# Optimization experiments

Hardware: AMD Instinct MI355X
Metric: run time of the kernel (lower is better)

The kernel has to match this reference:

```python
import jax, jax.numpy as jnp
import numpy as np

NUM_SPEC_CHARS = 2  # matches init_kwargs
VOCAB = 50000
EMBED = 128
B = 4096

def setup_inputs() -> dict:
    key = jax.random.key(0)
    k1, k2 = jax.random.split(key)
    input_ = jax.random.normal(k1, (B, VOCAB - NUM_SPEC_CHARS), dtype=jnp.float32)
    word2vecs = jax.random.normal(k2, (VOCAB, EMBED), dtype=jnp.float32)
    return {"input_": input_, "word2vecs": word2vecs}

def reference(input_, word2vecs):
    # forward: matmul of (b, vocab_eff) against table with special chars stripped
    table = word2vecs[:-NUM_SPEC_CHARS] if NUM_SPEC_CHARS > 0 else word2vecs
    return jnp.matmul(input_, table)  # (b, embed)
```

## Files before the change

kernel.cpp:

```cpp
#include <hip/hip_runtime.h>

#define M_ROWS 4096
#define K_EFF  49998
#define K_PAD  50048
#define N_EMB  128
#define BM     64
#define BK     64
#define S_SPLIT 16
#define IT_TOTAL 782
#define OUT_ELEMS (M_ROWS * N_EMB)

typedef __attribute__((ext_vector_type(8))) short        short8;
typedef __attribute__((ext_vector_type(4))) float        floatx4;
typedef __attribute__((ext_vector_type(2))) float        floatx2;
typedef __attribute__((ext_vector_type(4))) unsigned int uintx4;

__device__ __forceinline__ unsigned short f2bf(float f){
  unsigned int u = __builtin_bit_cast(unsigned int, f);
  u += 0x7fffu + ((u >> 16) & 1u);
  return (unsigned short)(u >> 16);
}

__global__ void prep_bt(const float* __restrict__ W,
                        unsigned short* __restrict__ Bt,
                        float* __restrict__ out){
  __shared__ unsigned short T[64 * 132];
  const int tid = threadIdx.x;

  const int gid = blockIdx.x * 256 + tid;
  if (gid < OUT_ELEMS / 4) ((floatx4*)out)[gid] = (floatx4)0.0f;

  const int kp0 = blockIdx.x * 64;

#pragma unroll
  for (int p = 0; p < 8; ++p){
    const int id = p * 256 + tid;
    const int r  = id >> 5;
    const int c4 = id & 31;
    const int kp = kp0 + r;
    floatx4 f = (floatx4)0.0f;
    if (kp < K_EFF) f = *(const floatx4*)(W + (size_t)kp * N_EMB + c4 * 4);
    const unsigned int u0 = f2bf(f.x) | ((unsigned)f2bf(f.y) << 16);
    const unsigned int u1 = f2bf(f.z) | ((unsigned)f2bf(f.w) << 16);
    *(unsigned int*)(&T[r * 132 + c4 * 4])     = u0;
    *(unsigned int*)(&T[r * 132 + c4 * 4 + 2]) = u1;
  }
  __syncthreads();

#pragma unroll
  for (int p = 0; p < 4; ++p){
    const int id = p * 256 + tid;
    const int n  = id >> 3;
    const int c  = id & 7;
    unsigned short v[8];
#pragma unroll
    for (int j = 0; j < 8; ++j) v[j] = T[(c * 8 + j) * 132 + n];
    uintx4 pk;
    pk.x = v[0] | ((unsigned)v[1] << 16);
    pk.y = v[2] | ((unsigned)v[3] << 16);
    pk.z = v[4] | ((unsigned)v[5] << 16);
    pk.w = v[6] | ((unsigned)v[7] << 16);
    *(uintx4*)(Bt + (size_t)n * K_PAD + kp0 + c * 8) = pk;
  }
}

__global__ void gemm_bf16_splitk(const float* __restrict__ A,
                                 const unsigned short* __restrict__ Bt,
                                 float* __restrict__ out){
  __shared__ unsigned short As[BM * 72];
  __shared__ unsigned short Bs[N_EMB * 72];

  const int tid   = threadIdx.x;
  const int bx    = blockIdx.x;
  const int mtile = bx & 63;
  const int s     = bx >> 6;
  const int m0    = mtile * BM;
  const int it0   = (s * IT_TOTAL) >> 4;
  const int it1   = ((s + 1) * IT_TOTAL) >> 4;

  const int lane = tid & 63;
  const int wv   = tid >> 6;
  const int col  = lane & 15;
  const int quad = lane >> 4;

  floatx4 acc[8];
#pragma unroll
  for (int c = 0; c < 8; ++c) acc[c] = (floatx4)0.0f;

  for (int it = it0; it < it1; ++it){
    const int kt = it * BK;
    __syncthreads();

    if (kt + BK <= K_EFF){
#pragma unroll
      for (int p = 0; p < 2; ++p){
        const int row = p * 32 + (tid >> 3);
        const int c   = tid & 7;
        const floatx2* src =
            (const floatx2*)(A + (size_t)(m0 + row) * K_EFF + kt + c * 8);
        floatx2 f0 = __builtin_nontemporal_load(src + 0);
        floatx2 f1 = __builtin_nontemporal_load(src + 1);
        floatx2 f2 = __builtin_nontemporal_load(src + 2);
        floatx2 f3 = __builtin_nontemporal_load(src + 3);
        uintx4 pk;
        pk.x = f2bf(f0.x) | ((unsigned)f2bf(f0.y) << 16);
        pk.y = f2bf(f1.x) | ((unsigned)f2bf(f1.y) << 16);
        pk.z = f2bf(f2.x) | ((unsigned)f2bf(f2.y) << 16);
        pk.w = f2bf(f3.x) | ((unsigned)f2bf(f3.y) << 16);
        *(uintx4*)(&As[row * 72 + c * 8]) = pk;
      }
    } else {
#pragma unroll
      for (int p = 0; p < 2; ++p){
        const int row = p * 32 + (tid >> 3);
        const int c   = tid & 7;
        const float* src = A + (size_t)(m0 + row) * K_EFF;
        unsigned short v[8];
#pragma unroll
        for (int j = 0; j < 8; ++j){
          const int k = kt + c * 8 + j;
          v[j] = (k < K_EFF) ? f2bf(src[k]) : (unsigned short)0;
        }
        uintx4 pk;
        pk.x = v[0] | ((unsigned)v[1] << 16);
        pk.y = v[2] | ((unsigned)v[3] << 16);
        pk.z = v[4] | ((unsigned)v[5] << 16);
        pk.w = v[6] | ((unsigned)v[7] << 16);
        *(uintx4*)(&As[row * 72 + c * 8]) = pk;
      }
    }

#pragma unroll
    for (int p = 0; p < 4; ++p){
      const int n = p * 32 + (tid >> 3);
      const int c = tid & 7;
      const uintx4 d = *(const uintx4*)(Bt + (size_t)n * K_PAD + kt + c * 8);
      *(uintx4*)(&Bs[n * 72 + c * 8]) = d;
    }
    __syncthreads();

#pragma unroll
    for (int ks = 0; ks < BK; ks += 32){
      const short8 af =
          *(const short8*)(&As[(16 * wv + col) * 72 + ks + quad * 8]);
#pragma unroll
      for (int c = 0; c < 8; ++c){
        const short8 bf =
            *(const short8*)(&Bs[(16 * c + col) * 72 + ks + quad * 8]);
        acc[c] = __builtin_amdgcn_mfma_f32_16x16x32_bf16(af, bf, acc[c], 0, 0, 0);
      }
    }
  }

  const int rbase = m0 + 16 * wv + quad * 4;
#pragma unroll
  for (int c = 0; c < 8; ++c){
#pragma unroll
    for (int i = 0; i < 4; ++i){
      atomicAdd(out + (size_t)(rbase + i) * N_EMB + 16 * c + col, acc[c][i]);
    }
  }
}

extern "C" void kernel_launch(void* const* d_in, const int* in_sizes, int n_in,
                              void* d_out, int out_size, void* d_ws, size_t ws_size,
                              hipStream_t stream) {
  const float* A = (const float*)d_in[0];
  const float* W = (const float*)d_in[1];
  float* out = (float*)d_out;
  unsigned short* Bt = (unsigned short*)d_ws;

  prep_bt<<<dim3(K_PAD / 64), dim3(256), 0, stream>>>(W, Bt, out);
  gemm_bf16_splitk<<<dim3(64 * S_SPLIT), dim3(256), 0, stream>>>(A, Bt, out);
}
```

Measured before the change: 1.153 ms.

## Load A directly into MFMA registers and stream B via global_load_lds with swizzle

```diff
diff --git a/kernel.cpp b/kernel.cpp
--- a/kernel.cpp
+++ b/kernel.cpp
@@ -40,10 +40,8 @@
     const int kp = kp0 + r;
     floatx4 f = (floatx4)0.0f;
     if (kp < K_EFF) f = *(const floatx4*)(W + (size_t)kp * N_EMB + c4 * 4);
-    const unsigned int u0 = f2bf(f.x) | ((unsigned)f2bf(f.y) << 16);
-    const unsigned int u1 = f2bf(f.z) | ((unsigned)f2bf(f.w) << 16);
-    *(unsigned int*)(&T[r * 132 + c4 * 4])     = u0;
-    *(unsigned int*)(&T[r * 132 + c4 * 4 + 2]) = u1;
+    *(unsigned int*)(&T[r * 132 + c4 * 4])     = f2bf(f.x) | ((unsigned)f2bf(f.y) << 16);
+    *(unsigned int*)(&T[r * 132 + c4 * 4 + 2]) = f2bf(f.z) | ((unsigned)f2bf(f.w) << 16);
   }
   __syncthreads();
 
@@ -64,11 +62,11 @@
   }
 }
 
-__global__ void gemm_bf16_splitk(const float* __restrict__ A,
-                                 const unsigned short* __restrict__ Bt,
-                                 float* __restrict__ out){
-  __shared__ unsigned short As[BM * 72];
-  __shared__ unsigned short Bs[N_EMB * 72];
+__global__ __launch_bounds__(256, 4)
+void gemm_bf16_splitk(const float* __restrict__ A,
+                      const unsigned short* __restrict__ Bt,
+                      float* __restrict__ out){
+  __shared__ __align__(16) unsigned short Bs[N_EMB * BK];
 
   const int tid   = threadIdx.x;
   const int bx    = blockIdx.x;
@@ -82,6 +80,12 @@
   const int wv   = tid >> 6;
   const int col  = lane & 15;
   const int quad = lane >> 4;
+  const int x    = col & 7;
+
+  const int sl = (lane & 7) ^ (lane >> 3);
+  const int nr = lane >> 3;
+
+  const float* Arow = A + (size_t)(m0 + 16 * wv + col) * K_EFF;
 
   floatx4 acc[8];
 #pragma unroll
@@ -91,62 +95,53 @@
     const int kt = it * BK;
     __syncthreads();
 
+#pragma unroll
+    for (int p = 0; p < 4; ++p){
+      const int n = (p * 4 + wv) * 8 + nr;
+      const unsigned short* g = Bt + (size_t)n * K_PAD + kt + sl * 8;
+      __builtin_amdgcn_global_load_lds(
+          (const __attribute__((address_space(1))) void*)g,
+          (__attribute__((address_space(3))) void*)(Bs + (p * 4 + wv) * 512),
+          16, 0, 0);
+    }
+
+    float a[16];
     if (kt + BK <= K_EFF){
+      const floatx2* ap = (const floatx2*)(Arow + kt + quad * 8);
+      const floatx2* aq = (const floatx2*)(Arow + kt + 32 + quad * 8);
 #pragma unroll
-      for (int p = 0; p < 2; ++p){
-        const int row = p * 32 + (tid >> 3);
-        const int c   = tid & 7;
-        const floatx2* src =
-            (const floatx2*)(A + (size_t)(m0 + row) * K_EFF + kt + c * 8);
-        floatx2 f0 = __builtin_nontemporal_load(src + 0);
-        floatx2 f1 = __builtin_nontemporal_load(src + 1);
-        floatx2 f2 = __builtin_nontemporal_load(src + 2);
-        floatx2 f3 = __builtin_nontemporal_load(src + 3);
-        uintx4 pk;
-        pk.x = f2bf(f0.x) | ((unsigned)f2bf(f0.y) << 16);
-        pk.y = f2bf(f1.x) | ((unsigned)f2bf(f1.y) << 16);
-        pk.z = f2bf(f2.x) | ((unsigned)f2bf(f2.y) << 16);
-        pk.w = f2bf(f3.x) | ((unsigned)f2bf(f3.y) << 16);
-        *(uintx4*)(&As[row * 72 + c * 8]) = pk;
+      for (int h = 0; h < 4; ++h){
+        floatx2 u = __builtin_nontemporal_load(ap + h);
+        floatx2 v = __builtin_nontemporal_load(aq + h);
+        a[2 * h] = u.x; a[2 * h + 1] = u.y;
+        a[8 + 2 * h] = v.x; a[8 + 2 * h + 1] = v.y;
       }
     } else {
 #pragma unroll
-      for (int p = 0; p < 2; ++p){
-        const int row = p * 32 + (tid >> 3);
-        const int c   = tid & 7;
-        const float* src = A + (size_t)(m0 + row) * K_EFF;
-        unsigned short v[8];
-#pragma unroll
-        for (int j = 0; j < 8; ++j){
-          const int k = kt + c * 8 + j;
-          v[j] = (k < K_EFF) ? f2bf(src[k]) : (unsigned short)0;
-        }
-        uintx4 pk;
-        pk.x = v[0] | ((unsigned)v[1] << 16);
-        pk.y = v[2] | ((unsigned)v[3] << 16);
-        pk.z = v[4] | ((unsigned)v[5] << 16);
-        pk.w = v[6] | ((unsigned)v[7] << 16);
-        *(uintx4*)(&As[row * 72 + c * 8]) = pk;
+      for (int j = 0; j < 8; ++j){
+        const int k0 = kt + quad * 8 + j;
+        const int k1 = k0 + 32;
+        a[j]     = (k0 < K_EFF) ? Arow[k0] : 0.0f;
+        a[8 + j] = (k1 < K_EFF) ? Arow[k1] : 0.0f;
       }
     }
+    short8 af0, af1;
+#pragma unroll
+    for (int j = 0; j < 8; ++j){
+      af0[j] = (short)f2bf(a[j]);
+      af1[j] = (short)f2bf(a[8 + j]);
+    }
 
-#pragma unroll
-    for (int p = 0; p < 4; ++p){
-      const int n = p * 32 + (tid >> 3);
-      const int c = tid & 7;
-      const uintx4 d = *(const uintx4*)(Bt + (size_t)n * K_PAD + kt + c * 8);
-      *(uintx4*)(&Bs[n * 72 + c * 8]) = d;
-    }
     __syncthreads();
 
 #pragma unroll
-    for (int ks = 0; ks < BK; ks += 32){
-      const short8 af =
-          *(const short8*)(&As[(16 * wv + col) * 72 + ks + quad * 8]);
+    for (int ks = 0; ks < 2; ++ks){
+      const short8 af = ks ? af1 : af0;
+      const int kc = ks * 4 + quad;
 #pragma unroll
       for (int c = 0; c < 8; ++c){
-        const short8 bf =
-            *(const short8*)(&Bs[(16 * c + col) * 72 + ks + quad * 8]);
+        const int n = 16 * c + col;
+        const short8 bf = *(const short8*)(Bs + n * 64 + ((kc ^ x) << 3));
         acc[c] = __builtin_amdgcn_mfma_f32_16x16x32_bf16(af, bf, acc[c], 0, 0, 0);
       }
     }
```

New measurement: 1.192 ms. +3.4%, slower.
